# Kernel optimization log

Measured on AMD Instinct MI355X. Metric: run time of the kernel, lower is better.

The kernel has to match this reference:

```python
import jax, jax.numpy as jnp
import numpy as np
import math

SCALED = True
SUBSEQUENT_MASK = True
B, SQ, SK, D, DV = 8, 2048, 2048, 1024, 1024


def _build_mask(query_lens, key_lens, sq, sk, causal):
    # (B, Sq, Sk) boolean validity mask: rows >= q_len and cols >= k_len are masked.
    qm = jnp.arange(sq)[None, :, None] < query_lens[:, None, None]
    km = jnp.arange(sk)[None, None, :] < key_lens[:, None, None]
    mask = qm & km
    if causal:
        mask = mask & (jnp.arange(sk)[None, None, :] <= jnp.arange(sq)[None, :, None])
    return mask


def _masked_softmax(scores, mask):
    # Stable masked softmax; fully-masked rows yield exactly 0 (matches the
    # original's NaN -> 0 replacement) without producing NaNs.
    neg = jnp.finfo(scores.dtype).min
    s = jnp.where(mask, scores, neg)
    m = jnp.max(s, axis=-1, keepdims=True)
    e = jnp.where(mask, jnp.exp(s - m), jnp.zeros((), scores.dtype))
    denom = jnp.sum(e, axis=-1, keepdims=True)
    return e / jnp.where(denom == 0, jnp.ones((), scores.dtype), denom)


def setup_inputs() -> dict:
    key = jax.random.key(0)
    kq, kk, kv, kql, kkl = jax.random.split(key, 5)
    return {
        "queries": jax.random.normal(kq, (B, SQ, D), dtype=jnp.float32),
        "keys": jax.random.normal(kk, (B, SK, D), dtype=jnp.float32),
        "values": jax.random.normal(kv, (B, SK, DV), dtype=jnp.float32),
        "query_lens": jax.random.randint(kql, (B,), 1, SQ + 1),
        "key_lens": jax.random.randint(kkl, (B,), 1, SK + 1),
    }


def reference(queries, keys, values, query_lens, key_lens):
    # scores: (B, Sq, Sk)
    scores = jnp.einsum("bqd,bkd->bqk", queries, keys)
    if SCALED:
        scores = scores / math.sqrt(queries.shape[2])
    mask = _build_mask(query_lens, key_lens, queries.shape[1], keys.shape[1], SUBSEQUENT_MASK)
    weights = _masked_softmax(scores, mask)
    context = jnp.einsum("bqk,bkv->bqv", weights, values)
    return (context, weights)
```

## Files before the change

### kernel.cpp

```cpp
#include <hip/hip_runtime.h>
#include <hip/hip_bf16.h>

#define B_   8
#define SQ_  2048
#define SK_  2048
#define D_   1024
#define DV_  1024

typedef __bf16 bf16;
typedef __attribute__((ext_vector_type(4))) __bf16 bf16x4;
typedef __attribute__((ext_vector_type(8))) __bf16 bf16x8;
typedef __attribute__((ext_vector_type(4))) float  f32x4;

typedef const __attribute__((address_space(1))) void* gptr1;
typedef __attribute__((address_space(3))) void*       lptr3;

__device__ __forceinline__ void gload16(const void* g, void* l) {
    __builtin_amdgcn_global_load_lds((gptr1)g, (lptr3)l, 16, 0, 0);
}

__global__ __launch_bounds__(256)
void convert_kernel(const float* __restrict__ A, const float* __restrict__ Bm,
                    bf16* __restrict__ dA, bf16* __restrict__ dB,
                    float* __restrict__ rowsumG)
{
    if (rowsumG && blockIdx.y == 0 && blockIdx.x < 8) {
        int idx = blockIdx.x * 256 + threadIdx.x;
        float4 z = make_float4(0.f, 0.f, 0.f, 0.f);
        ((float4*)rowsumG)[idx * 2 + 0] = z;
        ((float4*)rowsumG)[idx * 2 + 1] = z;
    }
    const float* src = blockIdx.y ? Bm : A;
    bf16*        dst = blockIdx.y ? dB : dA;
    size_t i = ((size_t)blockIdx.x * 256 + threadIdx.x) * 8;
    float4 v0 = *(const float4*)(src + i);
    float4 v1 = *(const float4*)(src + i + 4);
    bf16x8 o = { (bf16)v0.x, (bf16)v0.y, (bf16)v0.z, (bf16)v0.w,
                 (bf16)v1.x, (bf16)v1.y, (bf16)v1.z, (bf16)v1.w };
    *(bf16x8*)(dst + i) = o;
}

__global__ __launch_bounds__(256)
void convVT_kernel(const float* __restrict__ V, bf16* __restrict__ VT)
{
    const int b  = blockIdx.z;
    const int k0 = blockIdx.x * 64;
    const int n0 = blockIdx.y * 64;
    __shared__ bf16 T[64][72];

    const int tid = threadIdx.x;
    #pragma unroll
    for (int i = 0; i < 4; ++i) {
        int s  = tid + i * 256;
        int r  = s >> 4;
        int c4 = (s & 15) << 2;
        float4 v = *(const float4*)(V + ((size_t)b * SK_ + (k0 + r)) * DV_ + n0 + c4);
        T[r][c4 + 0] = (bf16)v.x;
        T[r][c4 + 1] = (bf16)v.y;
        T[r][c4 + 2] = (bf16)v.z;
        T[r][c4 + 3] = (bf16)v.w;
    }
    __syncthreads();
    #pragma unroll
    for (int i = 0; i < 2; ++i) {
        int s  = tid + i * 256;
        int n  = s >> 3;
        int c8 = (s & 7) << 3;
        bf16x8 o;
        #pragma unroll
        for (int j = 0; j < 8; ++j) o[j] = T[c8 + j][n];
        *(bf16x8*)(VT + ((size_t)b * DV_ + (n0 + n)) * SK_ + k0 + c8) = o;
    }
}

__global__ __launch_bounds__(512, 4)
void attnP_kernel(const bf16* __restrict__ Qbf, const bf16* __restrict__ Kbf,
                  const int* __restrict__ qlens, const int* __restrict__ klens,
                  bf16* __restrict__ Wbf, float* __restrict__ rowsumG)
{
    const int v    = blockIdx.x & 255;
    const int inst = blockIdx.x >> 8;
    const int b    = v & 7;
    const int s    = v >> 3;
    const int qs   = inst ? (31 - s) : s;
    const int par  = inst;
    const int q0   = qs * 64;
    const int qlen = qlens[b], klen = klens[b];
    if (q0 >= qlen) return;

    const int ncols  = min(klen, q0 + 64);
    const int ktiles = (ncols + 127) >> 7;

    __shared__ __align__(16) bf16 Qs[2][64][64];
    __shared__ __align__(16) bf16 Ks[2][128][64];
    __shared__ float rowsum[64];

    const int tid  = threadIdx.x;
    const int lane = tid & 63;
    const int w    = tid >> 6;

    if (tid < 64) rowsum[tid] = 0.f;

    const bf16* Qb = Qbf + ((size_t)b * SQ_ + q0) * (size_t)D_;
    const bf16* Kb = Kbf + (size_t)b * SK_ * (size_t)D_;
    bf16* Wrow0 = Wbf + ((size_t)b * SQ_ + q0) * SK_;

    const int r0 = tid >> 3;
    const int c0 = (tid & 7) << 3;
    const int g  = lane >> 4;
    const int cl = lane & 15;

    for (int kt = par; kt < ktiles; kt += 2) {
        const bf16* Kt = Kb + (size_t)(kt * 128) * (size_t)D_;
        gload16(Qb + (size_t)r0 * D_ + c0,        &Qs[0][r0][c0]);
        gload16(Kt + (size_t)r0 * D_ + c0,        &Ks[0][r0][c0]);
        gload16(Kt + (size_t)(r0 + 64) * D_ + c0, &Ks[0][r0 + 64][c0]);
        __syncthreads();

        f32x4 acc[4] = {};
        for (int dc = 0; dc < 16; ++dc) {
            const int cur = dc & 1;
            if (dc < 15) {
                const int d1 = (dc + 1) * 64;
                gload16(Qb + (size_t)r0 * D_ + d1 + c0,        &Qs[cur ^ 1][r0][c0]);
                gload16(Kt + (size_t)r0 * D_ + d1 + c0,        &Ks[cur ^ 1][r0][c0]);
                gload16(Kt + (size_t)(r0 + 64) * D_ + d1 + c0, &Ks[cur ^ 1][r0 + 64][c0]);
            }
            #pragma unroll
            for (int st = 0; st < 2; ++st) {
                const int koff = st * 32 + (g << 3);
                bf16x8 bb = *(const bf16x8*)&Ks[cur][16 * w + cl][koff];
                #pragma unroll
                for (int t = 0; t < 4; ++t) {
                    bf16x8 a = *(const bf16x8*)&Qs[cur][16 * t + cl][koff];
                    acc[t] = __builtin_amdgcn_mfma_f32_16x16x32_bf16(a, bb, acc[t], 0, 0, 0);
                }
            }
            __syncthreads();
        }

        const int colg = kt * 128 + 16 * w + cl;
        #pragma unroll
        for (int t = 0; t < 4; ++t) {
            #pragma unroll
            for (int r = 0; r < 4; ++r) {
                const int rl   = 16 * t + 4 * g + r;
                const int rowg = q0 + rl;
                float e = 0.f;
                if (rowg < qlen && colg <= rowg && colg < klen)
                    e = __expf(acc[t][r] * 0.03125f);
                Wrow0[(size_t)rl * SK_ + colg] = (bf16)e;
                float esum = e;
                esum += __shfl_xor(esum, 1, 64);
                esum += __shfl_xor(esum, 2, 64);
                esum += __shfl_xor(esum, 4, 64);
                esum += __shfl_xor(esum, 8, 64);
                if (cl == 0) atomicAdd(&rowsum[rl], esum);
            }
        }
    }

    __syncthreads();
    if (tid < 64) {
        float sv = rowsum[tid];
        if (sv > 0.f) atomicAdd(&rowsumG[(size_t)b * SQ_ + q0 + tid], sv);
    }
}

__global__ __launch_bounds__(512)
void normW_kernel(const int* __restrict__ qlens, const int* __restrict__ klens,
                  const float* __restrict__ rowsumG, bf16* __restrict__ Wbf,
                  float* __restrict__ W, float* __restrict__ invG)
{
    const int b  = blockIdx.y;
    const int q0 = blockIdx.x * 64;
    const int qlen = qlens[b], klen = klens[b];
    const int tid = threadIdx.x;
    float* Wb = W + ((size_t)b * SQ_ + q0) * SK_;

    if (q0 >= qlen) {
        float4 z = make_float4(0.f, 0.f, 0.f, 0.f);
        float4* wf = (float4*)Wb;
        #pragma unroll
        for (int i = 0; i < 64; ++i) wf[tid + i * 512] = z;
        float4* bfp = (float4*)(Wbf + ((size_t)b * SQ_ + q0) * SK_);
        #pragma unroll
        for (int i = 0; i < 32; ++i) bfp[tid + i * 512] = z;
        if (tid < 64) invG[(size_t)b * SQ_ + q0 + tid] = 0.f;
        return;
    }

    const int ncols = min(klen, q0 + 64);
    const int kendB = ((ncols + 127) >> 7) << 7;

    __shared__ float invS[64];
    if (tid < 64) {
        float sv = rowsumG[(size_t)b * SQ_ + q0 + tid];
        float iv = (sv > 0.f) ? (1.f / sv) : 0.f;
        invS[tid] = iv;
        invG[(size_t)b * SQ_ + q0 + tid] = iv;
    }
    __syncthreads();

    const int r  = tid >> 3;
    const int c8 = tid & 7;
    const float iv = invS[r];
    const bf16* Erow = Wbf + ((size_t)b * SQ_ + q0 + r) * SK_;
    float* Wrow = Wb + (size_t)r * SK_;
    for (int j = 0; j < 64; ++j) {
        int col = (c8 + j * 8) << 2;
        float4 o;
        if (col < kendB) {
            bf16x4 e4 = *(const bf16x4*)&Erow[col];
            o = make_float4((float)e4[0] * iv, (float)e4[1] * iv,
                            (float)e4[2] * iv, (float)e4[3] * iv);
        } else {
            o = make_float4(0.f, 0.f, 0.f, 0.f);
        }
        *(float4*)&Wrow[col] = o;
    }
}

__global__ __launch_bounds__(512, 4)
void context_bf_kernel(const bf16* __restrict__ Wbf, const bf16* __restrict__ VT,
                       const int* __restrict__ qlens, const int* __restrict__ klens,
                       const float* __restrict__ invG, float* __restrict__ Out)
{
    const int b  = blockIdx.z;
    const int q0 = blockIdx.y * 128;
    const int n0 = blockIdx.x * 128;
    const int tid  = threadIdx.x;
    const int qlen = qlens[b];

    float* Ob = Out + (size_t)b * SQ_ * DV_;
    if (q0 >= qlen) {
        float4 z = make_float4(0.f, 0.f, 0.f, 0.f);
        #pragma unroll
        for (int i = 0; i < 8; ++i) {
            int s  = tid + i * 512;
            int r  = s >> 5;
            int c4 = (s & 31) << 2;
            *(float4*)(Ob + (size_t)(q0 + r) * DV_ + n0 + c4) = z;
        }
        return;
    }

    const int klen = klens[b];
    const int kend = min(q0 + 128, (klen + 63) & ~63);
    const int nk   = kend >> 6;

    __shared__ __align__(16) bf16 Ws[2][128][64];
    __shared__ __align__(16) bf16 Vs[2][128][64];

    const int lane = tid & 63;
    const int w    = tid >> 6;
    const int wq   = w >> 1, wn = w & 1;

    const bf16* Wb = Wbf + (size_t)b * SQ_ * SK_ + (size_t)q0 * SK_;
    const bf16* Vb = VT  + (size_t)b * DV_ * SK_ + (size_t)n0 * SK_;

    const int r0 = tid >> 3;
    const int c0 = (tid & 7) << 3;

    auto stage = [&](int buf, int kk0) {
        gload16(Wb + (size_t)r0 * SK_ + kk0 + c0,        &Ws[buf][r0][c0]);
        gload16(Wb + (size_t)(r0 + 64) * SK_ + kk0 + c0, &Ws[buf][r0 + 64][c0]);
        gload16(Vb + (size_t)r0 * SK_ + kk0 + c0,        &Vs[buf][r0][c0]);
        gload16(Vb + (size_t)(r0 + 64) * SK_ + kk0 + c0, &Vs[buf][r0 + 64][c0]);
    };

    f32x4 acc[2][4] = {};

    stage(0, 0);
    __syncthreads();

    for (int it = 0; it < nk; ++it) {
        const int cur = it & 1;
        if (it + 1 < nk) stage(cur ^ 1, (it + 1) * 64);
        #pragma unroll
        for (int kk = 0; kk < 2; ++kk) {
            const int koff = kk * 32 + ((lane >> 4) << 3);
            bf16x8 a[2], bb[4];
            #pragma unroll
            for (int m = 0; m < 2; ++m)
                a[m] = *(const bf16x8*)&Ws[cur][32 * wq + 16 * m + (lane & 15)][koff];
            #pragma unroll
            for (int n = 0; n < 4; ++n)
                bb[n] = *(const bf16x8*)&Vs[cur][64 * wn + 16 * n + (lane & 15)][koff];
            #pragma unroll
            for (int m = 0; m < 2; ++m)
                #pragma unroll
                for (int n = 0; n < 4; ++n)
                    acc[m][n] = __builtin_amdgcn_mfma_f32_16x16x32_bf16(a[m], bb[n], acc[m][n], 0, 0, 0);
        }
        __syncthreads();
    }

    const float* invB = invG + (size_t)b * SQ_;
    const int rb = q0 + 32 * wq + ((lane >> 4) << 2);
    const int cb = n0 + 64 * wn + (lane & 15);
    #pragma unroll
    for (int m = 0; m < 2; ++m) {
        #pragma unroll
        for (int r = 0; r < 4; ++r) {
            const float iv = invB[rb + 16 * m + r];
            #pragma unroll
            for (int n = 0; n < 4; ++n)
                Ob[(size_t)(rb + 16 * m + r) * DV_ + (cb + 16 * n)] = acc[m][n][r] * iv;
        }
    }
}

__global__ __launch_bounds__(512, 4)
void scores_kernel(const float* __restrict__ Q, const float* __restrict__ K,
                   const int* __restrict__ qlens, const int* __restrict__ klens,
                   float* __restrict__ Wout)
{
    const int b  = blockIdx.z;
    const int q0 = blockIdx.y * 128;
    const int k0 = blockIdx.x * 128;
    if (k0 > q0 + 127) return;
    const int qlen = qlens[b], klen = klens[b];
    if (q0 >= qlen || k0 >= klen) return;

    __shared__ __align__(16) bf16 Qs[2][128][72];
    __shared__ __align__(16) bf16 Ks[2][128][72];

    const int tid  = threadIdx.x;
    const int lane = tid & 63;
    const int w    = tid >> 6;
    const int wq   = w >> 1, wk = w & 1;

    const float* Qb = Q + (size_t)b * SQ_ * D_;
    const float* Kb = K + (size_t)b * SK_ * D_;

    float4 qreg[4], kreg[4];
    int srow[4], sc4[4];
    #pragma unroll
    for (int i = 0; i < 4; ++i) {
        int s = tid + i * 512;
        srow[i] = s >> 4;
        sc4[i]  = (s & 15) << 2;
    }

    auto load_tile = [&](int d0) {
        #pragma unroll
        for (int i = 0; i < 4; ++i) {
            qreg[i] = *(const float4*)(Qb + (size_t)(q0 + srow[i]) * D_ + d0 + sc4[i]);
            kreg[i] = *(const float4*)(Kb + (size_t)(k0 + srow[i]) * D_ + d0 + sc4[i]);
        }
    };
    auto store_tile = [&](int buf) {
        #pragma unroll
        for (int i = 0; i < 4; ++i) {
            bf16x4 qb = { (bf16)qreg[i].x, (bf16)qreg[i].y, (bf16)qreg[i].z, (bf16)qreg[i].w };
            bf16x4 kb = { (bf16)kreg[i].x, (bf16)kreg[i].y, (bf16)kreg[i].z, (bf16)kreg[i].w };
            *(bf16x4*)&Qs[buf][srow[i]][sc4[i]] = qb;
            *(bf16x4*)&Ks[buf][srow[i]][sc4[i]] = kb;
        }
    };

    f32x4 acc[2][4] = {};
    load_tile(0);
    store_tile(0);
    __syncthreads();

    for (int it = 0; it < 16; ++it) {
        const int cur = it & 1;
        if (it < 15) load_tile((it + 1) * 64);
        #pragma unroll
        for (int kk = 0; kk < 2; ++kk) {
            const int koff = kk * 32 + ((lane >> 4) << 3);
            bf16x8 a[2], bb[4];
            #pragma unroll
            for (int m = 0; m < 2; ++m)
                a[m] = *(const bf16x8*)&Qs[cur][32 * wq + 16 * m + (lane & 15)][koff];
            #pragma unroll
            for (int n = 0; n < 4; ++n)
                bb[n] = *(const bf16x8*)&Ks[cur][64 * wk + 16 * n + (lane & 15)][koff];
            #pragma unroll
            for (int m = 0; m < 2; ++m)
                #pragma unroll
                for (int n = 0; n < 4; ++n)
                    acc[m][n] = __builtin_amdgcn_mfma_f32_16x16x32_bf16(a[m], bb[n], acc[m][n], 0, 0, 0);
        }
        if (it < 15) store_tile(1 - cur);
        __syncthreads();
    }

    float* Wb = Wout + (size_t)b * SQ_ * SK_;
    const int rb = q0 + 32 * wq + ((lane >> 4) << 2);
    const int cb = k0 + 64 * wk + (lane & 15);
    #pragma unroll
    for (int m = 0; m < 2; ++m)
        #pragma unroll
        for (int n = 0; n < 4; ++n)
            #pragma unroll
            for (int r = 0; r < 4; ++r)
                Wb[(size_t)(rb + 16 * m + r) * SK_ + (cb + 16 * n)] = acc[m][n][r] * 0.03125f;
}

__global__ __launch_bounds__(256)
void softmax_kernel(const int* __restrict__ qlens, const int* __restrict__ klens,
                    float* __restrict__ W)
{
    const int bq = blockIdx.x;
    const int b  = bq >> 11;
    const int q  = bq & 2047;
    const int qlen = qlens[b], klen = klens[b];
    int kmax = 0;
    if (q < qlen) kmax = min(klen, q + 1);

    float4* row = (float4*)(W + (size_t)bq * SK_);
    const int tid = threadIdx.x;

    float4 x[2];
    float m = -INFINITY;
    #pragma unroll
    for (int i = 0; i < 2; ++i) {
        int v4 = tid + i * 256;
        int kb = v4 << 2;
        if (kb < kmax) x[i] = row[v4];
        else           x[i] = make_float4(-INFINITY, -INFINITY, -INFINITY, -INFINITY);
        float* xe = (float*)&x[i];
        #pragma unroll
        for (int e = 0; e < 4; ++e) {
            if (kb + e >= kmax) xe[e] = -INFINITY;
            m = fmaxf(m, xe[e]);
        }
    }
    #pragma unroll
    for (int off = 32; off > 0; off >>= 1) m = fmaxf(m, __shfl_xor(m, off, 64));
    __shared__ float red[4];
    if ((tid & 63) == 0) red[tid >> 6] = m;
    __syncthreads();
    m = fmaxf(fmaxf(red[0], red[1]), fmaxf(red[2], red[3]));
    __syncthreads();

    float sum = 0.f;
    #pragma unroll
    for (int i = 0; i < 2; ++i) {
        float* xe = (float*)&x[i];
        #pragma unroll
        for (int e = 0; e < 4; ++e) {
            float ev = (xe[e] == -INFINITY) ? 0.f : __expf(xe[e] - m);
            xe[e] = ev;
            sum += ev;
        }
    }
    #pragma unroll
    for (int off = 32; off > 0; off >>= 1) sum += __shfl_xor(sum, off, 64);
    if ((tid & 63) == 0) red[tid >> 6] = sum;
    __syncthreads();
    sum = red[0] + red[1] + red[2] + red[3];

    const float inv = (sum > 0.f) ? (1.f / sum) : 0.f;
    #pragma unroll
    for (int i = 0; i < 2; ++i) {
        float* xe = (float*)&x[i];
        float4 o = { xe[0] * inv, xe[1] * inv, xe[2] * inv, xe[3] * inv };
        row[tid + i * 256] = o;
    }
}

__global__ __launch_bounds__(512, 4)
void context_kernel(const float* __restrict__ W, const float* __restrict__ V,
                    const int* __restrict__ klens, float* __restrict__ Out)
{
    const int b  = blockIdx.z;
    const int q0 = blockIdx.y * 128;
    const int n0 = blockIdx.x * 128;
    const int klen = klens[b];
    const int kend = min(q0 + 128, (klen + 63) & ~63);
    const int nk   = kend >> 6;

    __shared__ __align__(16) bf16 Ws[2][128][72];
    __shared__ __align__(16) bf16 Vs[2][128][72];

    const int tid  = threadIdx.x;
    const int lane = tid & 63;
    const int w    = tid >> 6;
    const int wq   = w >> 1, wn = w & 1;

    const float* Wb = W + (size_t)b * SQ_ * SK_;
    const float* Vb = V + (size_t)b * SK_ * DV_;

    float4 wreg[4];
    float  vreg[2][8];
    int srow[4], sc4[4], vn[2], voct[2];
    #pragma unroll
    for (int i = 0; i < 4; ++i) {
        int s = tid + i * 512;
        srow[i] = s >> 4;
        sc4[i]  = (s & 15) << 2;
    }
    #pragma unroll
    for (int i = 0; i < 2; ++i) {
        int t = tid + i * 512;
        vn[i]   = t & 127;
        voct[i] = t >> 7;
    }

    auto load_tile = [&](int kk0) {
        #pragma unroll
        for (int i = 0; i < 4; ++i)
            wreg[i] = *(const float4*)(Wb + (size_t)(q0 + srow[i]) * SK_ + kk0 + sc4[i]);
        #pragma unroll
        for (int i = 0; i < 2; ++i)
            #pragma unroll
            for (int j = 0; j < 8; ++j)
                vreg[i][j] = Vb[(size_t)(kk0 + voct[i] * 8 + j) * DV_ + n0 + vn[i]];
    };
    auto store_tile = [&](int buf) {
        #pragma unroll
        for (int i = 0; i < 4; ++i) {
            bf16x4 wb = { (bf16)wreg[i].x, (bf16)wreg[i].y, (bf16)wreg[i].z, (bf16)wreg[i].w };
            *(bf16x4*)&Ws[buf][srow[i]][sc4[i]] = wb;
        }
        #pragma unroll
        for (int i = 0; i < 2; ++i) {
            bf16x8 vb = { (bf16)vreg[i][0], (bf16)vreg[i][1], (bf16)vreg[i][2], (bf16)vreg[i][3],
                          (bf16)vreg[i][4], (bf16)vreg[i][5], (bf16)vreg[i][6], (bf16)vreg[i][7] };
            *(bf16x8*)&Vs[buf][vn[i]][voct[i] * 8] = vb;
        }
    };

    f32x4 acc[2][4] = {};
    load_tile(0);
    store_tile(0);
    __syncthreads();

    for (int it = 0; it < nk; ++it) {
        const int cur = it & 1;
        if (it + 1 < nk) load_tile((it + 1) * 64);
        #pragma unroll
        for (int kk = 0; kk < 2; ++kk) {
            const int koff = kk * 32 + ((lane >> 4) << 3);
            bf16x8 a[2], bb[4];
            #pragma unroll
            for (int m = 0; m < 2; ++m)
                a[m] = *(const bf16x8*)&Ws[cur][32 * wq + 16 * m + (lane & 15)][koff];
            #pragma unroll
            for (int n = 0; n < 4; ++n)
                bb[n] = *(const bf16x8*)&Vs[cur][64 * wn + 16 * n + (lane & 15)][koff];
            #pragma unroll
            for (int m = 0; m < 2; ++m)
                #pragma unroll
                for (int n = 0; n < 4; ++n)
                    acc[m][n] = __builtin_amdgcn_mfma_f32_16x16x32_bf16(a[m], bb[n], acc[m][n], 0, 0, 0);
        }
        if (it + 1 < nk) store_tile(1 - cur);
        __syncthreads();
    }

    float* Ob = Out + (size_t)b * SQ_ * DV_;
    const int rb = q0 + 32 * wq + ((lane >> 4) << 2);
    const int cb = n0 + 64 * wn + (lane & 15);
    #pragma unroll
    for (int m = 0; m < 2; ++m)
        #pragma unroll
        for (int n = 0; n < 4; ++n)
            #pragma unroll
            for (int r = 0; r < 4; ++r)
                Ob[(size_t)(rb + 16 * m + r) * DV_ + (cb + 16 * n)] = acc[m][n][r];
}

extern "C" void kernel_launch(void* const* d_in, const int* in_sizes, int n_in,
                              void* d_out, int out_size, void* d_ws, size_t ws_size,
                              hipStream_t stream) {
    (void)in_sizes; (void)n_in; (void)out_size;
    const float* Q     = (const float*)d_in[0];
    const float* K     = (const float*)d_in[1];
    const float* V     = (const float*)d_in[2];
    const int*   qlens = (const int*)d_in[3];
    const int*   klens = (const int*)d_in[4];

    float* ctx = (float*)d_out;
    float* wts = ctx + (size_t)B_ * SQ_ * DV_;

    const size_t nQ = (size_t)B_ * SQ_ * D_;
    const size_t nK = (size_t)B_ * SK_ * D_;
    const size_t nV = (size_t)B_ * SK_ * DV_;
    const size_t nW = (size_t)B_ * SQ_ * SK_;
    const size_t nS = (size_t)B_ * SQ_;
    const size_t ws_need = (nQ + nK + nV + nW) * sizeof(bf16) + nS * 2 * sizeof(float);

    if (d_ws && ws_size >= ws_need) {
        bf16*  qbf = (bf16*)d_ws;
        bf16*  kbf = qbf + nQ;
        bf16*  vbt = kbf + nK;
        bf16*  wbf = vbt + nV;
        float* rowsumG = (float*)(wbf + nW);
        float* invG    = rowsumG + nS;

        convert_kernel<<<dim3((unsigned)(nQ / (256 * 8)), 2), 256, 0, stream>>>(Q, K, qbf, kbf, rowsumG);
        convVT_kernel<<<dim3(SK_ / 64, DV_ / 64, B_), 256, 0, stream>>>(V, vbt);

        attnP_kernel<<<dim3(512), 512, 0, stream>>>(qbf, kbf, qlens, klens, wbf, rowsumG);

        normW_kernel<<<dim3(SQ_ / 64, B_), 512, 0, stream>>>(qlens, klens, rowsumG, wbf, wts, invG);

        dim3 g3(DV_ / 128, SQ_ / 128, B_);
        context_bf_kernel<<<g3, 512, 0, stream>>>(wbf, vbt, qlens, klens, invG, ctx);
    } else {
        dim3 g1(SK_ / 128, SQ_ / 128, B_);
        scores_kernel<<<g1, 512, 0, stream>>>(Q, K, qlens, klens, wts);

        softmax_kernel<<<dim3(B_ * SQ_), 256, 0, stream>>>(qlens, klens, wts);

        dim3 g3(DV_ / 128, SQ_ / 128, B_);
        context_kernel<<<g3, 512, 0, stream>>>(wts, V, klens, ctx);
    }
}
```

Baseline: 550.7 us.

## Retile scores into a 2D grid of 128x128 blocks and drop context double-buffering

Replaces the persistent 64-row attnP scores kernel, which looped over key tiles per block, with a 3D-grid kernel. In the new kernel each block computes one 128x128 causal tile of exp(QK^T), with eight waves arranged 4x2 over the tile. This raises parallelism and per-tile operand reuse. Row sums are reduced into shared memory and then atomically added to global memory. The context kernel's LDS double buffering is also removed, presumably to lower shared memory use. The cost is that global loads are no longer overlapped with MFMA work in either kernel.

```diff
diff --git a/kernel.cpp b/kernel.cpp
--- a/kernel.cpp
+++ b/kernel.cpp
@@ -74,96 +74,93 @@
 }
 
 __global__ __launch_bounds__(512, 4)
-void attnP_kernel(const bf16* __restrict__ Qbf, const bf16* __restrict__ Kbf,
-                  const int* __restrict__ qlens, const int* __restrict__ klens,
-                  bf16* __restrict__ Wbf, float* __restrict__ rowsumG)
-{
-    const int v    = blockIdx.x & 255;
-    const int inst = blockIdx.x >> 8;
-    const int b    = v & 7;
-    const int s    = v >> 3;
-    const int qs   = inst ? (31 - s) : s;
-    const int par  = inst;
-    const int q0   = qs * 64;
+void scoresE_kernel(const bf16* __restrict__ Qbf, const bf16* __restrict__ Kbf,
+                    const int* __restrict__ qlens, const int* __restrict__ klens,
+                    bf16* __restrict__ Wbf, float* __restrict__ rowsumG)
+{
+    const int b  = blockIdx.z;
+    const int q0 = blockIdx.y * 128;
+    const int k0 = blockIdx.x * 128;
+    if (k0 > q0 + 127) return;
     const int qlen = qlens[b], klen = klens[b];
-    if (q0 >= qlen) return;
-
-    const int ncols  = min(klen, q0 + 64);
-    const int ktiles = (ncols + 127) >> 7;
-
-    __shared__ __align__(16) bf16 Qs[2][64][64];
-    __shared__ __align__(16) bf16 Ks[2][128][64];
-    __shared__ float rowsum[64];
+    if (q0 >= qlen || k0 >= klen) return;
+
+    __shared__ __align__(16) bf16 Qs[128][64];
+    __shared__ __align__(16) bf16 Ks[128][64];
+    __shared__ float rowsumL[128];
 
     const int tid  = threadIdx.x;
     const int lane = tid & 63;
     const int w    = tid >> 6;
-
-    if (tid < 64) rowsum[tid] = 0.f;
-
-    const bf16* Qb = Qbf + ((size_t)b * SQ_ + q0) * (size_t)D_;
-    const bf16* Kb = Kbf + (size_t)b * SK_ * (size_t)D_;
-    bf16* Wrow0 = Wbf + ((size_t)b * SQ_ + q0) * SK_;
+    const int wq   = w >> 1, wk = w & 1;
+
+    if (tid < 128) rowsumL[tid] = 0.f;
+
+    const bf16* Qb = Qbf + ((size_t)b * SQ_ + q0) * D_;
+    const bf16* Kb = Kbf + ((size_t)b * SK_ + k0) * D_;
 
     const int r0 = tid >> 3;
     const int c0 = (tid & 7) << 3;
-    const int g  = lane >> 4;
-    const int cl = lane & 15;
-
-    for (int kt = par; kt < ktiles; kt += 2) {
-        const bf16* Kt = Kb + (size_t)(kt * 128) * (size_t)D_;
-        gload16(Qb + (size_t)r0 * D_ + c0,        &Qs[0][r0][c0]);
-        gload16(Kt + (size_t)r0 * D_ + c0,        &Ks[0][r0][c0]);
-        gload16(Kt + (size_t)(r0 + 64) * D_ + c0, &Ks[0][r0 + 64][c0]);
+
+    f32x4 acc[2][4] = {};
+
+    for (int d0 = 0; d0 < D_; d0 += 64) {
+        gload16(Qb + (size_t)r0 * D_ + d0 + c0,        &Qs[r0][c0]);
+        gload16(Qb + (size_t)(r0 + 64) * D_ + d0 + c0, &Qs[r0 + 64][c0]);
+        gload16(Kb + (size_t)r0 * D_ + d0 + c0,        &Ks[r0][c0]);
+        gload16(Kb + (size_t)(r0 + 64) * D_ + d0 + c0, &Ks[r0 + 64][c0]);
         __syncthreads();
-
-        f32x4 acc[4] = {};
-        for (int dc = 0; dc < 16; ++dc) {
-            const int cur = dc & 1;
-            if (dc < 15) {
-                const int d1 = (dc + 1) * 64;
-                gload16(Qb + (size_t)r0 * D_ + d1 + c0,        &Qs[cur ^ 1][r0][c0]);
-                gload16(Kt + (size_t)r0 * D_ + d1 + c0,        &Ks[cur ^ 1][r0][c0]);
-                gload16(Kt + (size_t)(r0 + 64) * D_ + d1 + c0, &Ks[cur ^ 1][r0 + 64][c0]);
-            }
-            #pragma unroll
-            for (int st = 0; st < 2; ++st) {
-                const int koff = st * 32 + (g << 3);
-                bf16x8 bb = *(const bf16x8*)&Ks[cur][16 * w + cl][koff];
+        #pragma unroll
+        for (int kk = 0; kk < 2; ++kk) {
+            const int koff = kk * 32 + ((lane >> 4) << 3);
+            bf16x8 a[2], bb[4];
+            #pragma unroll
+            for (int m = 0; m < 2; ++m)
+                a[m] = *(const bf16x8*)&Qs[32 * wq + 16 * m + (lane & 15)][koff];
+            #pragma unroll
+            for (int n = 0; n < 4; ++n)
+                bb[n] = *(const bf16x8*)&Ks[64 * wk + 16 * n + (lane & 15)][koff];
+            #pragma unroll
+            for (int m = 0; m < 2; ++m)
                 #pragma unroll
-                for (int t = 0; t < 4; ++t) {
-                    bf16x8 a = *(const bf16x8*)&Qs[cur][16 * t + cl][koff];
-                    acc[t] = __builtin_amdgcn_mfma_f32_16x16x32_bf16(a, bb, acc[t], 0, 0, 0);
-                }
-            }
-            __syncthreads();
-        }
-
-        const int colg = kt * 128 + 16 * w + cl;
-        #pragma unroll
-        for (int t = 0; t < 4; ++t) {
-            #pragma unroll
-            for (int r = 0; r < 4; ++r) {
-                const int rl   = 16 * t + 4 * g + r;
-                const int rowg = q0 + rl;
+                for (int n = 0; n < 4; ++n)
+                    acc[m][n] = __builtin_amdgcn_mfma_f32_16x16x32_bf16(a[m], bb[n], acc[m][n], 0, 0, 0);
+        }
+        __syncthreads();
+    }
+
+    bf16* Wrow = Wbf + ((size_t)b * SQ_ + q0) * SK_ + k0;
+    const int g   = lane >> 4;
+    const int cl  = lane & 15;
+    const int rbl = 32 * wq + (g << 2);
+    const int cbl = 64 * wk + cl;
+    #pragma unroll
+    for (int m = 0; m < 2; ++m) {
+        #pragma unroll
+        for (int r = 0; r < 4; ++r) {
+            const int rl   = rbl + 16 * m + r;
+            const int rowg = q0 + rl;
+            float s = 0.f;
+            #pragma unroll
+            for (int n = 0; n < 4; ++n) {
+                const int colg = k0 + cbl + 16 * n;
                 float e = 0.f;
                 if (rowg < qlen && colg <= rowg && colg < klen)
-                    e = __expf(acc[t][r] * 0.03125f);
-                Wrow0[(size_t)rl * SK_ + colg] = (bf16)e;
-                float esum = e;
-                esum += __shfl_xor(esum, 1, 64);
-                esum += __shfl_xor(esum, 2, 64);
-                esum += __shfl_xor(esum, 4, 64);
-                esum += __shfl_xor(esum, 8, 64);
-                if (cl == 0) atomicAdd(&rowsum[rl], esum);
+                    e = __expf(acc[m][n][r] * 0.03125f);
+                Wrow[(size_t)rl * SK_ + cbl + 16 * n] = (bf16)e;
+                s += e;
             }
-        }
-    }
-
-    __syncthreads();
-    if (tid < 64) {
-        float sv = rowsum[tid];
-        if (sv > 0.f) atomicAdd(&rowsumG[(size_t)b * SQ_ + q0 + tid], sv);
+            s += __shfl_xor(s, 1, 64);
+            s += __shfl_xor(s, 2, 64);
+            s += __shfl_xor(s, 4, 64);
+            s += __shfl_xor(s, 8, 64);
+            if (cl == 0) atomicAdd(&rowsumL[rl], s);
+        }
+    }
+    __syncthreads();
+    if (tid < 128) {
+        float sv = rowsumL[tid];
+        if (sv != 0.f) atomicAdd(&rowsumG[(size_t)b * SQ_ + q0 + tid], sv);
     }
 }
 
@@ -249,8 +246,8 @@
     const int kend = min(q0 + 128, (klen + 63) & ~63);
     const int nk   = kend >> 6;
 
-    __shared__ __align__(16) bf16 Ws[2][128][64];
-    __shared__ __align__(16) bf16 Vs[2][128][64];
+    __shared__ __align__(16) bf16 Ws[128][64];
+    __shared__ __align__(16) bf16 Vs[128][64];
 
     const int lane = tid & 63;
     const int w    = tid >> 6;
@@ -262,31 +259,25 @@
     const int r0 = tid >> 3;
     const int c0 = (tid & 7) << 3;
 
-    auto stage = [&](int buf, int kk0) {
-        gload16(Wb + (size_t)r0 * SK_ + kk0 + c0,        &Ws[buf][r0][c0]);
-        gload16(Wb + (size_t)(r0 + 64) * SK_ + kk0 + c0, &Ws[buf][r0 + 64][c0]);
-        gload16(Vb + (size_t)r0 * SK_ + kk0 + c0,        &Vs[buf][r0][c0]);
-        gload16(Vb + (size_t)(r0 + 64) * SK_ + kk0 + c0, &Vs[buf][r0 + 64][c0]);
-    };
-
     f32x4 acc[2][4] = {};
 
-    stage(0, 0);
-    __syncthreads();
-
     for (int it = 0; it < nk; ++it) {
-        const int cur = it & 1;
-        if (it + 1 < nk) stage(cur ^ 1, (it + 1) * 64);
+        const int kk0 = it * 64;
+        gload16(Wb + (size_t)r0 * SK_ + kk0 + c0,        &Ws[r0][c0]);
+        gload16(Wb + (size_t)(r0 + 64) * SK_ + kk0 + c0, &Ws[r0 + 64][c0]);
+        gload16(Vb + (size_t)r0 * SK_ + kk0 + c0,        &Vs[r0][c0]);
+        gload16(Vb + (size_t)(r0 + 64) * SK_ + kk0 + c0, &Vs[r0 + 64][c0]);
+        __syncthreads();
         #pragma unroll
         for (int kk = 0; kk < 2; ++kk) {
             const int koff = kk * 32 + ((lane >> 4) << 3);
             bf16x8 a[2], bb[4];
             #pragma unroll
             for (int m = 0; m < 2; ++m)
-                a[m] = *(const bf16x8*)&Ws[cur][32 * wq + 16 * m + (lane & 15)][koff];
+                a[m] = *(const bf16x8*)&Ws[32 * wq + 16 * m + (lane & 15)][koff];
             #pragma unroll
             for (int n = 0; n < 4; ++n)
-                bb[n] = *(const bf16x8*)&Vs[cur][64 * wn + 16 * n + (lane & 15)][koff];
+                bb[n] = *(const bf16x8*)&Vs[64 * wn + 16 * n + (lane & 15)][koff];
             #pragma unroll
             for (int m = 0; m < 2; ++m)
                 #pragma unroll
@@ -596,7 +587,8 @@
         convert_kernel<<<dim3((unsigned)(nQ / (256 * 8)), 2), 256, 0, stream>>>(Q, K, qbf, kbf, rowsumG);
         convVT_kernel<<<dim3(SK_ / 64, DV_ / 64, B_), 256, 0, stream>>>(V, vbt);
 
-        attnP_kernel<<<dim3(512), 512, 0, stream>>>(qbf, kbf, qlens, klens, wbf, rowsumG);
+        dim3 g1(SK_ / 128, SQ_ / 128, B_);
+        scoresE_kernel<<<g1, 512, 0, stream>>>(qbf, kbf, qlens, klens, wbf, rowsumG);
 
         normW_kernel<<<dim3(SQ_ / 64, B_), 512, 0, stream>>>(qlens, klens, rowsumG, wbf, wts, invG);
 
```

New measurement: 504.8 us. 1.09x faster.
